# Performance work log

Measured on AMD Instinct MI355X. Metric: run time of the kernel, lower is better.

Reference implementation:

```python
import jax, jax.numpy as jnp
import numpy as np

N_LEVELS = 16
N_FEAT = 2
LOG2_T = 19
T = 2 ** LOG2_T
BASE_RES = 2 ** 4
MAX_RES = 2 ** 11
PER_LEVEL_SCALE = np.exp((np.log(MAX_RES) - np.log(BASE_RES)) / (N_LEVELS - 1))
RESOLUTIONS = [int(np.floor(BASE_RES * PER_LEVEL_SCALE ** lv)) + 1 for lv in range(N_LEVELS)]
INIT_ACTIVE_LEVEL = 8
N_POINTS = 1048576
N_OUT = N_LEVELS * N_FEAT
# tcnn spatial hashing primes
P1 = jnp.uint32(2654435761)
P2 = jnp.uint32(805459861)


def _level_lookup(x, tbl, res):
    """x: [N,3] in [0,1], tbl: [T,F], res: python int grid resolution."""
    pos = x * (res - 1)                       # [N,3]
    c0 = jnp.clip(jnp.floor(pos).astype(jnp.int32), 0, res - 2)
    w = pos - c0.astype(pos.dtype)            # [N,3] trilinear fractions
    feats = jnp.zeros((x.shape[0], tbl.shape[-1]), dtype=tbl.dtype)
    dense = (res ** 3) <= T                   # static per level: dense grid vs hashed
    for dz in (0, 1):
        for dy in (0, 1):
            for dx in (0, 1):
                offs = jnp.array([dx, dy, dz], jnp.int32)
                c = c0 + offs                 # [N,3] corner int coords
                if dense:
                    idx = c[:, 0] + res * (c[:, 1] + res * c[:, 2])
                else:
                    cu = c.astype(jnp.uint32)
                    idx = ((cu[:, 0]) ^ (cu[:, 1] * P1) ^ (cu[:, 2] * P2)) & jnp.uint32(T - 1)
                    idx = idx.astype(jnp.int32)
                # trilinear corner weight: prod over axes of (w if offs==1 else 1-w)
                wc = jnp.prod(jnp.where(offs == 1, w, 1.0 - w), axis=-1)  # [N]
                feats = feats + tbl[idx] * wc[:, None]
    return feats


def setup_inputs() -> dict:
    key = jax.random.key(0)
    k1, k2 = jax.random.split(key)
    x = jax.random.uniform(k1, (N_POINTS, 3), dtype=jnp.float32)
    # tcnn-style small uniform init of the hash table
    table = jax.random.uniform(k2, (N_LEVELS, T, N_FEAT), dtype=jnp.float32,
                               minval=-1e-4, maxval=1e-4)
    mask = jnp.concatenate([
        jnp.ones(INIT_ACTIVE_LEVEL * N_FEAT, jnp.float32),
        jnp.zeros((N_LEVELS - INIT_ACTIVE_LEVEL) * N_FEAT, jnp.float32),
    ])
    return {"x": x, "table": table, "mask": mask}


def reference(x, table, mask):
    # multi-resolution hash grid encoding + progressive level mask
    outs = [_level_lookup(x, table[lv], RESOLUTIONS[lv]) for lv in range(N_LEVELS)]
    enc = jnp.concatenate(outs, axis=-1)      # [N, 32]
    return enc * mask
```

## Files before the change

### kernel.cpp

```cpp
#include <hip/hip_runtime.h>
#include <cstdint>
#include <cstddef>


namespace {

constexpr int      kNLevels = 16;
constexpr uint32_t kT       = 1u << 19;
constexpr uint32_t kP1      = 2654435761u;
constexpr uint32_t kP2      = 805459861u;

typedef float v2f __attribute__((ext_vector_type(2)));
typedef float v4f __attribute__((ext_vector_type(4)));

__device__ constexpr int kRes[kNLevels] = {
    17, 23, 31, 43, 59, 81, 112, 154, 213, 295, 407, 562, 777, 1073, 1483, 2049
};

__device__ inline void corner_setup(float px, float py, float pz, int res,
                                    int& cx, int& cy, int& cz,
                                    float& wx, float& wy, float& wz) {
    const float s = (float)(res - 1);
    const float fx = px * s, fy = py * s, fz = pz * s;
    cx = (int)floorf(fx); cy = (int)floorf(fy); cz = (int)floorf(fz);
    cx = min(max(cx, 0), res - 2);
    cy = min(max(cy, 0), res - 2);
    cz = min(max(cz, 0), res - 2);
    wx = fx - (float)cx; wy = fy - (float)cy; wz = fz - (float)cz;
}

__device__ inline void load_xyz(const float* __restrict__ x, int p,
                                float& px, float& py, float& pz) {
    float v[3];
    __builtin_memcpy(v, x + 3 * (size_t)p, 12);
    px = v[0]; py = v[1]; pz = v[2];
}

__global__ __launch_bounds__(256) void hashed_level_kernel(
    const float* __restrict__ x, const float* __restrict__ table,
    const float* __restrict__ mask, float* __restrict__ ws, int n)
{
    const int lv = 5 + blockIdx.y;
    const float m0 = mask[2 * lv], m1 = mask[2 * lv + 1];
    if (m0 == 0.0f && m1 == 0.0f) return;

    const int p = blockIdx.x * blockDim.x + threadIdx.x;
    if (p >= n) return;
    float px, py, pz;
    load_xyz(x, p, px, py, pz);

    const int res = kRes[lv];
    int cx, cy, cz; float wx, wy, wz;
    corner_setup(px, py, pz, res, cx, cy, cz, wx, wy, wz);
    const float ux = 1.0f - wx, uy = 1.0f - wy, uz = 1.0f - wz;
    const float* __restrict__ tbl = table + (size_t)lv * (size_t)(kT * 2);

    const uint32_t hy0 = (uint32_t)cy * kP1, hy1 = (uint32_t)(cy + 1) * kP1;
    const uint32_t hz0 = (uint32_t)cz * kP2, hz1 = (uint32_t)(cz + 1) * kP2;
    const uint32_t cxu = (uint32_t)cx;

    float r0 = 0.0f, r1 = 0.0f;
#pragma unroll
    for (int c = 0; c < 8; ++c) {
        const int dx = c & 1, dy = (c >> 1) & 1, dz = (c >> 2) & 1;
        const uint32_t idx =
            ((cxu + (uint32_t)dx) ^ (dy ? hy1 : hy0) ^ (dz ? hz1 : hz0))
            & (kT - 1u);
        const v2f v = *(const v2f*)(tbl + 2u * idx);
        const float w = (dx ? wx : ux) * (dy ? wy : uy) * (dz ? wz : uz);
        r0 = fmaf(v.x, w, r0);
        r1 = fmaf(v.y, w, r1);
    }
    v2f o; o.x = r0; o.y = r1;
    __builtin_nontemporal_store(
        o, (v2f*)(ws + ((size_t)(lv - 5) * n + p) * 2));
}

__global__ __launch_bounds__(256) void gather_out_kernel(
    const float* __restrict__ x, const float* __restrict__ table,
    const float* __restrict__ ws, const float* __restrict__ mask,
    float* __restrict__ out, int n)
{
    __shared__ float lds[256 * 32];

    const int tid = threadIdx.x;
    const int p   = blockIdx.x * 256 + tid;
    const int pc  = (p < n) ? p : (n - 1);

    float px, py, pz;
    load_xyz(x, pc, px, py, pz);

    v4f o[8];

#pragma unroll
    for (int lv = 5; lv < kNLevels; ++lv) {
        const float m0 = mask[2 * lv], m1 = mask[2 * lv + 1];
        float r0 = 0.0f, r1 = 0.0f;
        if (m0 != 0.0f || m1 != 0.0f) {
            const v2f v = __builtin_nontemporal_load(
                (const v2f*)(ws + ((size_t)(lv - 5) * n + pc) * 2));
            r0 = v.x * m0;
            r1 = v.y * m1;
        }
        if (lv & 1) { o[lv >> 1].z = r0; o[lv >> 1].w = r1; }
        else        { o[lv >> 1].x = r0; o[lv >> 1].y = r1; }
    }

#pragma unroll
    for (int lv = 0; lv < 5; ++lv) {
        const float m0 = mask[2 * lv], m1 = mask[2 * lv + 1];
        float r0 = 0.0f, r1 = 0.0f;
        if (m0 != 0.0f || m1 != 0.0f) {
            const int res = kRes[lv];
            int cx, cy, cz; float wx, wy, wz;
            corner_setup(px, py, pz, res, cx, cy, cz, wx, wy, wz);
            const float ux = 1.0f - wx, uy = 1.0f - wy, uz = 1.0f - wz;
            const float* __restrict__ tbl = table + (size_t)lv * (size_t)(kT * 2);
#pragma unroll
            for (int c = 0; c < 4; ++c) {
                const int dy = c & 1, dz = (c >> 1) & 1;
                const uint32_t idx0 =
                    (uint32_t)(cx + res * ((cy + dy) + res * (cz + dz)));
                v4f ab;
                __builtin_memcpy(&ab, tbl + 2u * idx0, sizeof(v4f));
                const float wyz = (dy ? wy : uy) * (dz ? wz : uz);
                const float w0 = ux * wyz, w1 = wx * wyz;
                r0 = fmaf(ab.x, w0, fmaf(ab.z, w1, r0));
                r1 = fmaf(ab.y, w0, fmaf(ab.w, w1, r1));
            }
            r0 *= m0; r1 *= m1;
        }
        if (lv & 1) { o[lv >> 1].z = r0; o[lv >> 1].w = r1; }
        else        { o[lv >> 1].x = r0; o[lv >> 1].y = r1; }
    }

#pragma unroll
    for (int c = 0; c < 8; ++c)
        *(v4f*)&lds[tid * 32 + ((c ^ (tid & 7)) << 2)] = o[c];
    __syncthreads();

    const long long bp = (long long)blockIdx.x * 256;
    float* const obase = out + (size_t)bp * 32;
#pragma unroll
    for (int j = 0; j < 8; ++j) {
        const int m  = tid + 256 * j;
        const int pr = m >> 3, c = m & 7;
        if (bp + pr < n) {
            const v4f v = *(const v4f*)&lds[pr * 32 + ((c ^ (pr & 7)) << 2)];
            __builtin_nontemporal_store(v, (v4f*)obase + m);
        }
    }
}

__global__ __launch_bounds__(256) void fused_kernel(
    const float* __restrict__ x, const float* __restrict__ table,
    const float* __restrict__ mask, float* __restrict__ out, int n)
{
    const int p = blockIdx.x * blockDim.x + threadIdx.x;
    if (p >= n) return;
    const float px = x[3 * p + 0], py = x[3 * p + 1], pz = x[3 * p + 2];
    v4f o[8];
#pragma unroll
    for (int lv = 0; lv < kNLevels; ++lv) {
        const float m0 = mask[2 * lv], m1 = mask[2 * lv + 1];
        float r0 = 0.0f, r1 = 0.0f;
        if (m0 != 0.0f || m1 != 0.0f) {
            const int res = kRes[lv];
            const bool dense = ((long long)res * res * res) <= (long long)kT;
            int cx, cy, cz; float wx, wy, wz;
            corner_setup(px, py, pz, res, cx, cy, cz, wx, wy, wz);
            const float ux = 1.0f - wx, uy = 1.0f - wy, uz = 1.0f - wz;
            const float* __restrict__ tbl = table + (size_t)lv * (size_t)(kT * 2);
#pragma unroll
            for (int c = 0; c < 8; ++c) {
                const int dx = c & 1, dy = (c >> 1) & 1, dz = (c >> 2) & 1;
                const int ix = cx + dx, iy = cy + dy, iz = cz + dz;
                uint32_t idx;
                if (dense) idx = (uint32_t)(ix + res * (iy + res * iz));
                else idx = (((uint32_t)ix) ^ ((uint32_t)iy * kP1)
                                           ^ ((uint32_t)iz * kP2)) & (kT - 1u);
                const v2f v = *(const v2f*)(tbl + 2u * idx);
                const float w = (dx ? wx : ux) * (dy ? wy : uy) * (dz ? wz : uz);
                r0 = fmaf(v.x, w, r0);
                r1 = fmaf(v.y, w, r1);
            }
            r0 *= m0; r1 *= m1;
        }
        if (lv & 1) { o[lv >> 1].z = r0; o[lv >> 1].w = r1; }
        else        { o[lv >> 1].x = r0; o[lv >> 1].y = r1; }
    }
    v4f* __restrict__ op = (v4f*)(out + (size_t)p * 32);
#pragma unroll
    for (int i = 0; i < 8; ++i) op[i] = o[i];
}

}

extern "C" void kernel_launch(void* const* d_in, const int* in_sizes, int n_in,
                              void* d_out, int out_size, void* d_ws, size_t ws_size,
                              hipStream_t stream) {
    const float* x     = (const float*)d_in[0];
    const float* table = (const float*)d_in[1];
    const float* mask  = (const float*)d_in[2];
    float*       out   = (float*)d_out;

    const int n = in_sizes[0] / 3;
    const int block = 256;
    const int gx = (n + block - 1) / block;

    const size_t ws_needed = (size_t)(kNLevels - 5) * (size_t)n * 2 * sizeof(float);
    if (ws_size >= ws_needed) {
        float* ws = (float*)d_ws;
        dim3 grid1(gx, kNLevels - 5);
        hashed_level_kernel<<<grid1, block, 0, stream>>>(x, table, mask, ws, n);
        gather_out_kernel<<<gx, block, 0, stream>>>(x, table, ws, mask, out, n);
    } else {
        fused_kernel<<<gx, block, 0, stream>>>(x, table, mask, out, n);
    }
}
```

Baseline: 325.1 us.

## Stage dense level 0-1 tables in LDS and widen gather blocks to 1024

The gather/output kernel now runs 1024-thread blocks. Each block copies the dense tables of levels 0 and 1 (about 136 KB) into LDS, interpolates those levels from LDS, and reuses the same buffer to stage the output tile. Levels 2-4 are computed without the mask branch. Separately, the hashed-level kernel issues all eight corner loads before doing any FMAs, to raise memory-level parallelism. The intent is to cut global gathers for the small dense levels, but every block re-reads the full tables from L2, and the large LDS footprint limits the CU to one 1024-thread block, which weakens latency hiding.

```diff
diff --git a/kernel.cpp b/kernel.cpp
--- a/kernel.cpp
+++ b/kernel.cpp
@@ -16,6 +16,11 @@
 __device__ constexpr int kRes[kNLevels] = {
     17, 23, 31, 43, 59, 81, 112, 154, 213, 295, 407, 562, 777, 1073, 1483, 2049
 };
+
+constexpr int kN0 = 17 * 17 * 17;
+constexpr int kN1 = 23 * 23 * 23;
+constexpr int kL1Base = kN0 + 1;
+constexpr int kLdsFloats = 34164;
 
 __device__ inline void corner_setup(float px, float py, float pz, int res,
                                     int& cx, int& cy, int& cz,
@@ -59,38 +64,78 @@
     const uint32_t hz0 = (uint32_t)cz * kP2, hz1 = (uint32_t)(cz + 1) * kP2;
     const uint32_t cxu = (uint32_t)cx;
 
-    float r0 = 0.0f, r1 = 0.0f;
+    v2f hv[8];
 #pragma unroll
     for (int c = 0; c < 8; ++c) {
         const int dx = c & 1, dy = (c >> 1) & 1, dz = (c >> 2) & 1;
         const uint32_t idx =
             ((cxu + (uint32_t)dx) ^ (dy ? hy1 : hy0) ^ (dz ? hz1 : hz0))
             & (kT - 1u);
-        const v2f v = *(const v2f*)(tbl + 2u * idx);
+        hv[c] = *(const v2f*)(tbl + 2u * idx);
+    }
+    float r0 = 0.0f, r1 = 0.0f;
+#pragma unroll
+    for (int c = 0; c < 8; ++c) {
+        const int dx = c & 1, dy = (c >> 1) & 1, dz = (c >> 2) & 1;
         const float w = (dx ? wx : ux) * (dy ? wy : uy) * (dz ? wz : uz);
-        r0 = fmaf(v.x, w, r0);
-        r1 = fmaf(v.y, w, r1);
+        r0 = fmaf(hv[c].x, w, r0);
+        r1 = fmaf(hv[c].y, w, r1);
     }
     v2f o; o.x = r0; o.y = r1;
     __builtin_nontemporal_store(
         o, (v2f*)(ws + ((size_t)(lv - 5) * n + p) * 2));
 }
 
-__global__ __launch_bounds__(256) void gather_out_kernel(
+__global__ __launch_bounds__(1024) void gather_out_kernel(
     const float* __restrict__ x, const float* __restrict__ table,
     const float* __restrict__ ws, const float* __restrict__ mask,
     float* __restrict__ out, int n)
 {
-    __shared__ float lds[256 * 32];
+    __shared__ float lds[kLdsFloats];
+    v2f* const tlds = (v2f*)lds;
 
     const int tid = threadIdx.x;
-    const int p   = blockIdx.x * 256 + tid;
-    const int pc  = (p < n) ? p : (n - 1);
+
+    {
+        const v2f* __restrict__ t0 = (const v2f*)table;
+        for (int e = tid; e < kN0; e += 1024) tlds[e] = t0[e];
+        const v2f* __restrict__ t1 = (const v2f*)(table + (size_t)(kT * 2));
+        for (int e = tid; e < kN1; e += 1024) tlds[kL1Base + e] = t1[e];
+    }
+
+    const int p  = blockIdx.x * 1024 + tid;
+    const int pc = (p < n) ? p : (n - 1);
 
     float px, py, pz;
     load_xyz(x, pc, px, py, pz);
 
     v4f o[8];
+
+#pragma unroll
+    for (int lv = 2; lv < 5; ++lv) {
+        const int res = kRes[lv];
+        int cx, cy, cz; float wx, wy, wz;
+        corner_setup(px, py, pz, res, cx, cy, cz, wx, wy, wz);
+        const float ux = 1.0f - wx, uy = 1.0f - wy, uz = 1.0f - wz;
+        const float* __restrict__ tbl = table + (size_t)lv * (size_t)(kT * 2);
+        const float m0 = mask[2 * lv], m1 = mask[2 * lv + 1];
+        float r0 = 0.0f, r1 = 0.0f;
+#pragma unroll
+        for (int c = 0; c < 4; ++c) {
+            const int dy = c & 1, dz = (c >> 1) & 1;
+            const uint32_t idx0 =
+                (uint32_t)(cx + res * ((cy + dy) + res * (cz + dz)));
+            v4f ab;
+            __builtin_memcpy(&ab, tbl + 2u * idx0, sizeof(v4f));
+            const float wyz = (dy ? wy : uy) * (dz ? wz : uz);
+            const float w0 = ux * wyz, w1 = wx * wyz;
+            r0 = fmaf(ab.x, w0, fmaf(ab.z, w1, r0));
+            r1 = fmaf(ab.y, w0, fmaf(ab.w, w1, r1));
+        }
+        r0 *= m0; r1 *= m1;
+        if (lv & 1) { o[lv >> 1].z = r0; o[lv >> 1].w = r1; }
+        else        { o[lv >> 1].x = r0; o[lv >> 1].y = r1; }
+    }
 
 #pragma unroll
     for (int lv = 5; lv < kNLevels; ++lv) {
@@ -106,44 +151,44 @@
         else        { o[lv >> 1].x = r0; o[lv >> 1].y = r1; }
     }
 
-#pragma unroll
-    for (int lv = 0; lv < 5; ++lv) {
-        const float m0 = mask[2 * lv], m1 = mask[2 * lv + 1];
-        float r0 = 0.0f, r1 = 0.0f;
-        if (m0 != 0.0f || m1 != 0.0f) {
-            const int res = kRes[lv];
-            int cx, cy, cz; float wx, wy, wz;
-            corner_setup(px, py, pz, res, cx, cy, cz, wx, wy, wz);
-            const float ux = 1.0f - wx, uy = 1.0f - wy, uz = 1.0f - wz;
-            const float* __restrict__ tbl = table + (size_t)lv * (size_t)(kT * 2);
-#pragma unroll
-            for (int c = 0; c < 4; ++c) {
-                const int dy = c & 1, dz = (c >> 1) & 1;
-                const uint32_t idx0 =
-                    (uint32_t)(cx + res * ((cy + dy) + res * (cz + dz)));
-                v4f ab;
-                __builtin_memcpy(&ab, tbl + 2u * idx0, sizeof(v4f));
-                const float wyz = (dy ? wy : uy) * (dz ? wz : uz);
-                const float w0 = ux * wyz, w1 = wx * wyz;
-                r0 = fmaf(ab.x, w0, fmaf(ab.z, w1, r0));
-                r1 = fmaf(ab.y, w0, fmaf(ab.w, w1, r1));
-            }
-            r0 *= m0; r1 *= m1;
-        }
-        if (lv & 1) { o[lv >> 1].z = r0; o[lv >> 1].w = r1; }
-        else        { o[lv >> 1].x = r0; o[lv >> 1].y = r1; }
-    }
-
+    __syncthreads();
+
+#pragma unroll
+    for (int lv = 0; lv < 2; ++lv) {
+        const int res  = kRes[lv];
+        const int base = lv ? kL1Base : 0;
+        const float m0 = mask[2 * lv], m1 = mask[2 * lv + 1];
+        int cx, cy, cz; float wx, wy, wz;
+        corner_setup(px, py, pz, res, cx, cy, cz, wx, wy, wz);
+        const float ux = 1.0f - wx, uy = 1.0f - wy, uz = 1.0f - wz;
+        float r0 = 0.0f, r1 = 0.0f;
+#pragma unroll
+        for (int c = 0; c < 4; ++c) {
+            const int dy = c & 1, dz = (c >> 1) & 1;
+            const int idx0 = cx + res * ((cy + dy) + res * (cz + dz));
+            const v2f a = tlds[base + idx0];
+            const v2f b = tlds[base + idx0 + 1];
+            const float wyz = (dy ? wy : uy) * (dz ? wz : uz);
+            const float w0 = ux * wyz, w1 = wx * wyz;
+            r0 = fmaf(a.x, w0, fmaf(b.x, w1, r0));
+            r1 = fmaf(a.y, w0, fmaf(b.y, w1, r1));
+        }
+        r0 *= m0; r1 *= m1;
+        if (lv & 1) { o[lv >> 1].z = r0; o[lv >> 1].w = r1; }
+        else        { o[lv >> 1].x = r0; o[lv >> 1].y = r1; }
+    }
+
+    __syncthreads();
 #pragma unroll
     for (int c = 0; c < 8; ++c)
         *(v4f*)&lds[tid * 32 + ((c ^ (tid & 7)) << 2)] = o[c];
     __syncthreads();
 
-    const long long bp = (long long)blockIdx.x * 256;
+    const long long bp = (long long)blockIdx.x * 1024;
     float* const obase = out + (size_t)bp * 32;
 #pragma unroll
     for (int j = 0; j < 8; ++j) {
-        const int m  = tid + 256 * j;
+        const int m  = tid + 1024 * j;
         const int pr = m >> 3, c = m & 7;
         if (bp + pr < n) {
             const v4f v = *(const v4f*)&lds[pr * 32 + ((c ^ (pr & 7)) << 2)];
@@ -213,7 +258,8 @@
         float* ws = (float*)d_ws;
         dim3 grid1(gx, kNLevels - 5);
         hashed_level_kernel<<<grid1, block, 0, stream>>>(x, table, mask, ws, n);
-        gather_out_kernel<<<gx, block, 0, stream>>>(x, table, ws, mask, out, n);
+        const int gx2 = (n + 1023) / 1024;
+        gather_out_kernel<<<gx2, 1024, 0, stream>>>(x, table, ws, mask, out, n);
     } else {
         fused_kernel<<<gx, block, 0, stream>>>(x, table, mask, out, n);
     }
```

New measurement: 330.9 us. Within noise of the previous version (+1.8%).
